# Kernel tuning notes

Hardware: AMD Instinct MI355X
Metric: run time of the kernel (lower is better)

## Reference

```python
import jax, jax.numpy as jnp
import numpy as np

B, N, MAX_DEG = 256, 512, 6
F_IN, H = 62, 128  # layers = [62, 128, 128]
NUM_DEG = MAX_DEG + 1  # degree buckets 0..6


def gather_neighbors(atoms, edges, maskvalue):
    # atoms [B,N,F], edges [B,N,D] with -1 padding -> [B,N,D,F]
    idx = jnp.maximum(edges, 0)
    neigh = jax.vmap(lambda a, e: a[e])(atoms, idx)
    return jnp.where(edges[..., None] < 0, jnp.asarray(maskvalue, atoms.dtype), neigh)


def nfp_conv(atoms, edges, W, b):
    # W [NUM_DEG, F_in, F_out], b [NUM_DEG, F_out]
    deg = jnp.sum(edges >= 0, axis=-1)  # [B,N]
    neigh = gather_neighbors(atoms, edges, 0.0)
    summed = neigh.sum(axis=2) + atoms  # include self, [B,N,F_in]
    out = jnp.zeros(summed.shape[:2] + (W.shape[-1],), summed.dtype)
    for d in range(NUM_DEG):  # small fixed set of degree buckets
        h = jax.nn.sigmoid(summed @ W[d] + b[d])
        out = out + h * (deg == d)[..., None].astype(h.dtype)
    return out


def graph_pool(atoms, edges):
    # max over self + neighbors
    neigh = gather_neighbors(atoms, edges, -jnp.inf)
    allf = jnp.concatenate([atoms[:, :, None, :], neigh], axis=2)  # [B,N,D+1,F]
    return allf.max(axis=2)


def setup_inputs() -> dict:
    key = jax.random.key(0)
    ka, ke, km, k0, k1, k2, k3 = jax.random.split(key, 7)
    a = jax.random.normal(ka, (B, N, F_IN), dtype=jnp.float32)
    e = jax.random.randint(ke, (B, N, MAX_DEG), 0, N, dtype=jnp.int32)
    # introduce -1 padding so atoms have varied degrees 0..6
    u = jax.random.uniform(km, (B, N, MAX_DEG))
    e = jnp.where(u < 0.6, e, -1).astype(jnp.int32)
    W0 = jax.random.normal(k0, (NUM_DEG, F_IN, H), dtype=jnp.float32) * 0.1
    b0 = jax.random.normal(k1, (NUM_DEG, H), dtype=jnp.float32) * 0.1
    W1 = jax.random.normal(k2, (NUM_DEG, H, H), dtype=jnp.float32) * 0.1
    b1 = jax.random.normal(k3, (NUM_DEG, H), dtype=jnp.float32) * 0.1
    return {"a": a, "e": e, "W0": W0, "b0": b0, "W1": W1, "b1": b1}


def reference(a, e, W0, b0, W1, b1):
    x = nfp_conv(a, e, W0, b0)
    x = graph_pool(x, e)
    x = nfp_conv(x, e, W1, b1)
    x = graph_pool(x, e)
    return x.sum(axis=1)  # SubgraphSum: [B, H]
```

## Files before the change

### kernel.cpp

```cpp
#include <hip/hip_runtime.h>
#include <math.h>

#define BB 256
#define NN 512
#define DD 6
#define F_IN 62
#define HH 128
#define ND 7
#define TOTAL (BB*NN)
#define OPB 640
#define GPB 40
#define TPB 10

typedef __bf16 bf16x8 __attribute__((ext_vector_type(8)));
typedef float f32x4 __attribute__((ext_vector_type(4)));

__device__ __forceinline__ unsigned short f2bf(float f) {
    unsigned u = __builtin_bit_cast(unsigned, f);
    u = (u + 0x7FFFu + ((u >> 16) & 1u)) >> 16;
    return (unsigned short)u;
}
__device__ __forceinline__ float lo2f(unsigned x) { return __builtin_bit_cast(float, x << 16); }
__device__ __forceinline__ float hi2f(unsigned x) { return __builtin_bit_cast(float, x & 0xFFFF0000u); }


__global__ __launch_bounds__(512) void k_sort16(const int* __restrict__ e,
                                                int* __restrict__ order,
                                                int* __restrict__ dgrp,
                                                int* __restrict__ ntiles) {
    __shared__ unsigned int scnt[ND];
    __shared__ unsigned int sbase[ND + 1];
    const int b = blockIdx.x;
    const int t = threadIdx.x;
    if (t < ND) scnt[t] = 0u;
    for (int i = t; i < OPB; i += 512) order[b * OPB + i] = -1;
    __syncthreads();
    int d = 0;
#pragma unroll
    for (int j = 0; j < DD; ++j) d += (e[(b * NN + t) * DD + j] >= 0) ? 1 : 0;
    unsigned rk = atomicAdd(&scnt[d], 1u);
    __syncthreads();
    if (t == 0) {
        unsigned acc = 0;
        for (int k = 0; k < ND; ++k) { sbase[k] = acc; acc += (scnt[k] + 15u) & ~15u; }
        sbase[ND] = acc;
        for (int k = 0; k < ND; ++k)
            for (unsigned g = sbase[k] >> 4; g < (sbase[k + 1] >> 4); ++g)
                dgrp[b * GPB + g] = k;
        for (unsigned g = acc >> 4; g < GPB; ++g) dgrp[b * GPB + g] = 0;
        ntiles[b] = (int)((acc + 63u) >> 6);
    }
    __syncthreads();
    order[b * OPB + sbase[d] + rk] = t;
}


__global__ __launch_bounds__(256) void k_prep_a(const float* __restrict__ a,
                                                unsigned short* __restrict__ Ap) {
    int u = blockIdx.x * 256 + threadIdx.x;
    int r = u >> 3;
    int c0 = (u & 7) * 8;
    unsigned short h[8];
#pragma unroll
    for (int i = 0; i < 8; ++i) {
        int c = c0 + i;
        h[i] = (c < F_IN) ? f2bf(a[(size_t)r * F_IN + c]) : (unsigned short)0;
    }
    uint4 p;
    p.x = (unsigned)h[0] | ((unsigned)h[1] << 16);
    p.y = (unsigned)h[2] | ((unsigned)h[3] << 16);
    p.z = (unsigned)h[4] | ((unsigned)h[5] << 16);
    p.w = (unsigned)h[6] | ((unsigned)h[7] << 16);
    *(uint4*)&Ap[(size_t)r * 64 + c0] = p;
}


__global__ void k_prep_wt(const float* __restrict__ W, unsigned short* __restrict__ WT,
                          int F, int K) {
    int n = blockIdx.x;
    int d = blockIdx.y;
    for (int k = threadIdx.x; k < K; k += 64) {
        float v = (k < F) ? W[((size_t)d * F + k) * HH + n] : 0.f;
        WT[((size_t)d * HH + n) * K + k] = f2bf(v);
    }
}


template<int KB>
__global__ __launch_bounds__(256, 3)
void k_conv_mfma(const unsigned short* __restrict__ Xp,
                 const int* __restrict__ e,
                 const unsigned short* __restrict__ WT,
                 const float* __restrict__ bias,
                 const int* __restrict__ order,
                 const int* __restrict__ dgrp,
                 const int* __restrict__ ntiles,
                 unsigned short* __restrict__ Y) {
    constexpr int K = KB * 8;
    constexpr int LOGKB = (KB == 16) ? 4 : 3;
    __shared__ unsigned short sP[64 * 128];
    __shared__ int vT[64];
    __shared__ int eT[64 * DD];

    const int t = threadIdx.x;
    const int l = t & 63;
    const int w = t >> 6;

    const int bi = blockIdx.x;
    const int x8 = bi & 7;
    const int j = bi >> 3;
    const int batch = x8 + 8 * (j / TPB);
    const int tile = j % TPB;
    if (tile >= ntiles[batch]) return;

    if (t < 64) vT[t] = order[batch * OPB + tile * 64 + t];
    __syncthreads();
    for (int i = t; i < 64 * DD; i += 256) {
        int v = vT[i / DD];
        if (v >= 0) eT[i] = e[((size_t)batch * NN + v) * DD + (i % DD)];
    }
    __syncthreads();

    for (int u = t; u < 64 * KB; u += 256) {
        const int kb = u & (KB - 1);
        const int n = u >> LOGKB;
        const int v = vT[n];
        float s[8] = {0.f, 0.f, 0.f, 0.f, 0.f, 0.f, 0.f, 0.f};
        if (v >= 0) {
            const unsigned short* base = Xp + (size_t)batch * NN * K;
            uint4 p = *(const uint4*)(base + (size_t)v * K + kb * 8);
            s[0] = lo2f(p.x); s[1] = hi2f(p.x); s[2] = lo2f(p.y); s[3] = hi2f(p.y);
            s[4] = lo2f(p.z); s[5] = hi2f(p.z); s[6] = lo2f(p.w); s[7] = hi2f(p.w);
#pragma unroll
            for (int jj = 0; jj < DD; ++jj) {
                int idx = eT[n * DD + jj];
                if (idx >= 0) {
                    uint4 q = *(const uint4*)(base + (size_t)idx * K + kb * 8);
                    s[0] += lo2f(q.x); s[1] += hi2f(q.x); s[2] += lo2f(q.y); s[3] += hi2f(q.y);
                    s[4] += lo2f(q.z); s[5] += hi2f(q.z); s[6] += lo2f(q.w); s[7] += hi2f(q.w);
                }
            }
        }
        uint4 r;
        r.x = (unsigned)f2bf(s[0]) | ((unsigned)f2bf(s[1]) << 16);
        r.y = (unsigned)f2bf(s[2]) | ((unsigned)f2bf(s[3]) << 16);
        r.z = (unsigned)f2bf(s[4]) | ((unsigned)f2bf(s[5]) << 16);
        r.w = (unsigned)f2bf(s[6]) | ((unsigned)f2bf(s[7]) << 16);
        const int kbs = kb ^ (n & 7);
        *(uint4*)&sP[(n * KB + kbs) * 8] = r;
    }
    __syncthreads();

    const int lr = l & 15;
    const int lq = l >> 4;

    int dg[4];
#pragma unroll
    for (int mb = 0; mb < 4; ++mb) dg[mb] = dgrp[batch * GPB + tile * 4 + mb];

    bf16x8 bf[K / 32][2];
    f32x4 acc[4][2];
    int dprev = -1;
#pragma unroll
    for (int mb = 0; mb < 4; ++mb) {
        const int d = dg[mb];
        if (d != dprev) {
#pragma unroll
            for (int kk = 0; kk < K / 32; ++kk)
#pragma unroll
                for (int nb = 0; nb < 2; ++nb) {
                    int ncol = w * 32 + nb * 16 + lr;
                    int krow = kk * 32 + lq * 8;
                    bf[kk][nb] = *(const bf16x8*)(WT + ((size_t)d * HH + ncol) * K + krow);
                }
            dprev = d;
        }
        f32x4 z0 = {0.f, 0.f, 0.f, 0.f};
        f32x4 z1 = {0.f, 0.f, 0.f, 0.f};
        const int nrow = mb * 16 + lr;
#pragma unroll
        for (int kk = 0; kk < K / 32; ++kk) {
            int kbp = kk * 4 + lq;
            int kbs = kbp ^ (nrow & 7);
            bf16x8 af = *(const bf16x8*)&sP[(nrow * KB + kbs) * 8];
            z0 = __builtin_amdgcn_mfma_f32_16x16x32_bf16(af, bf[kk][0], z0, 0, 0, 0);
            z1 = __builtin_amdgcn_mfma_f32_16x16x32_bf16(af, bf[kk][1], z1, 0, 0, 0);
        }
        acc[mb][0] = z0;
        acc[mb][1] = z1;
    }

    __syncthreads();
#pragma unroll
    for (int mb = 0; mb < 4; ++mb) {
        const int d = dg[mb];
#pragma unroll
        for (int nb = 0; nb < 2; ++nb) {
            int col = w * 32 + nb * 16 + lr;
            float bv = bias[d * HH + col];
#pragma unroll
            for (int r = 0; r < 4; ++r) {
                int n = mb * 16 + lq * 4 + r;
                float z = 1.f / (1.f + __expf(-(acc[mb][nb][r] + bv)));
                sP[n * HH + col] = f2bf(z);
            }
        }
    }
    __syncthreads();
    for (int u = t; u < 1024; u += 256) {
        int n = u >> 4;
        int c8 = (u & 15) * 8;
        int v = vT[n];
        if (v >= 0) {
            uint4 p = *(const uint4*)&sP[n * HH + c8];
            *(uint4*)&Y[((size_t)batch * NN + v) * HH + c8] = p;
        }
    }
}


__global__ __launch_bounds__(256) void k_pool_bf(const unsigned short* __restrict__ X,
                                                 const int* __restrict__ e,
                                                 unsigned short* __restrict__ P) {
    const int t = threadIdx.x;
    const int bi = blockIdx.x;
    const int x8 = bi & 7;
    const int j = bi >> 3;
    const int batch = x8 + 8 * (j >> 5);
    const int sub = j & 31;
    const int u = batch * NN + sub * 16 + (t >> 4);
    const int c8 = (t & 15) * 8;
    const int nbase = u & ~(NN - 1);
    float m[8];
    {
        uint4 p = *(const uint4*)(X + (size_t)u * HH + c8);
        m[0] = lo2f(p.x); m[1] = hi2f(p.x); m[2] = lo2f(p.y); m[3] = hi2f(p.y);
        m[4] = lo2f(p.z); m[5] = hi2f(p.z); m[6] = lo2f(p.w); m[7] = hi2f(p.w);
    }
#pragma unroll
    for (int jj = 0; jj < DD; ++jj) {
        int idx = e[u * DD + jj];
        if (idx >= 0) {
            uint4 p = *(const uint4*)(X + (size_t)(nbase + idx) * HH + c8);
            m[0] = fmaxf(m[0], lo2f(p.x)); m[1] = fmaxf(m[1], hi2f(p.x));
            m[2] = fmaxf(m[2], lo2f(p.y)); m[3] = fmaxf(m[3], hi2f(p.y));
            m[4] = fmaxf(m[4], lo2f(p.z)); m[5] = fmaxf(m[5], hi2f(p.z));
            m[6] = fmaxf(m[6], lo2f(p.w)); m[7] = fmaxf(m[7], hi2f(p.w));
        }
    }
    uint4 r;
    r.x = (unsigned)f2bf(m[0]) | ((unsigned)f2bf(m[1]) << 16);
    r.y = (unsigned)f2bf(m[2]) | ((unsigned)f2bf(m[3]) << 16);
    r.z = (unsigned)f2bf(m[4]) | ((unsigned)f2bf(m[5]) << 16);
    r.w = (unsigned)f2bf(m[6]) | ((unsigned)f2bf(m[7]) << 16);
    *(uint4*)&P[(size_t)u * HH + c8] = r;
}


__global__ __launch_bounds__(256) void k_pool_sum_part(const unsigned short* __restrict__ X,
                                                       const int* __restrict__ e,
                                                       float* __restrict__ partial) {
    __shared__ float red[16][HH + 4];
    const int t = threadIdx.x;
    const int bi = blockIdx.x;
    const int x8 = bi & 7;
    const int j = bi >> 3;
    const int b = x8 + 8 * (j >> 3);
    const int chunk = j & 7;
    const int slot = t >> 4;
    const int c8 = (t & 15) * 8;
    float acc[8];
#pragma unroll
    for (int i = 0; i < 8; ++i) acc[i] = 0.f;

    for (int n = chunk * 64 + slot; n < chunk * 64 + 64; n += 16) {
        int u = b * NN + n;
        float m[8];
        uint4 p = *(const uint4*)(X + (size_t)u * HH + c8);
        m[0] = lo2f(p.x); m[1] = hi2f(p.x); m[2] = lo2f(p.y); m[3] = hi2f(p.y);
        m[4] = lo2f(p.z); m[5] = hi2f(p.z); m[6] = lo2f(p.w); m[7] = hi2f(p.w);
#pragma unroll
        for (int jj = 0; jj < DD; ++jj) {
            int idx = e[u * DD + jj];
            if (idx >= 0) {
                uint4 q = *(const uint4*)(X + (size_t)(b * NN + idx) * HH + c8);
                m[0] = fmaxf(m[0], lo2f(q.x)); m[1] = fmaxf(m[1], hi2f(q.x));
                m[2] = fmaxf(m[2], lo2f(q.y)); m[3] = fmaxf(m[3], hi2f(q.y));
                m[4] = fmaxf(m[4], lo2f(q.z)); m[5] = fmaxf(m[5], hi2f(q.z));
                m[6] = fmaxf(m[6], lo2f(q.w)); m[7] = fmaxf(m[7], hi2f(q.w));
            }
        }
#pragma unroll
        for (int i = 0; i < 8; ++i) acc[i] += m[i];
    }
#pragma unroll
    for (int i = 0; i < 8; ++i) red[slot][c8 + i] = acc[i];
    __syncthreads();
    if (t < HH) {
        float s = 0.f;
#pragma unroll
        for (int k = 0; k < 16; ++k) s += red[k][t];
        partial[(size_t)(b * 8 + chunk) * HH + t] = s;
    }
}


__global__ __launch_bounds__(256) void k_sum_final(const float* __restrict__ partial,
                                                   float* __restrict__ out) {
    int g = blockIdx.x * 256 + threadIdx.x;
    int b = g >> 7;
    int c = g & 127;
    float s = 0.f;
#pragma unroll
    for (int k = 0; k < 8; ++k) s += partial[(size_t)(b * 8 + k) * HH + c];
    out[g] = s;
}


extern "C" void kernel_launch(void* const* d_in, const int* in_sizes, int n_in,
                              void* d_out, int out_size, void* d_ws, size_t ws_size,
                              hipStream_t stream) {
    const float* a  = (const float*)d_in[0];
    const int*   e  = (const int*)d_in[1];
    const float* W0 = (const float*)d_in[2];
    const float* b0 = (const float*)d_in[3];
    const float* W1 = (const float*)d_in[4];
    const float* b1 = (const float*)d_in[5];
    float* out = (float*)d_out;

    char* ws = (char*)d_ws;
    const size_t XB = (size_t)TOTAL * HH * 2;
    unsigned short* xbuf = (unsigned short*)ws;
    unsigned short* pbuf = (unsigned short*)(ws + XB);
    unsigned short* Ap   = (unsigned short*)(ws + 2 * XB);
    float* partial = (float*)Ap;
    unsigned short* WT0  = (unsigned short*)(ws + 2 * XB + (size_t)TOTAL * 64 * 2);
    unsigned short* WT1  = WT0 + (size_t)ND * HH * 64;
    char* ip = (char*)(WT1 + (size_t)ND * HH * 128);
    int* order  = (int*)ip;
    int* dgrp   = (int*)(ip + (size_t)BB * OPB * 4);
    int* ntiles = (int*)(ip + (size_t)BB * (OPB + GPB) * 4);

    hipLaunchKernelGGL(k_sort16, dim3(BB), dim3(NN), 0, stream, e, order, dgrp, ntiles);

    hipLaunchKernelGGL(k_prep_a, dim3(TOTAL * 8 / 256), dim3(256), 0, stream, a, Ap);
    hipLaunchKernelGGL(k_prep_wt, dim3(HH, ND), dim3(64), 0, stream, W0, WT0, F_IN, 64);
    hipLaunchKernelGGL(k_prep_wt, dim3(HH, ND), dim3(64), 0, stream, W1, WT1, HH, HH);

    hipLaunchKernelGGL((k_conv_mfma<8>),  dim3(BB * TPB), dim3(256), 0, stream,
                       Ap, e, WT0, b0, order, dgrp, ntiles, xbuf);
    hipLaunchKernelGGL(k_pool_bf, dim3(TOTAL / 16), dim3(256), 0, stream, xbuf, e, pbuf);
    hipLaunchKernelGGL((k_conv_mfma<16>), dim3(BB * TPB), dim3(256), 0, stream,
                       pbuf, e, WT1, b1, order, dgrp, ntiles, xbuf);
    hipLaunchKernelGGL(k_pool_sum_part, dim3(BB * 8), dim3(256), 0, stream, xbuf, e, partial);
    hipLaunchKernelGGL(k_sum_final, dim3(BB * HH / 256), dim3(256), 0, stream, partial, out);
}
```

Before: 146.5 us.

## Widen conv blocks to one wave per row-block slice and split pool-sum finer

The MFMA conv kernel now runs with 512 or 1024 threads per block. Each thread gathers exactly one neighbor-sum element, and each wave computes one 16-row block over a slice of output columns, with its A fragments preloaded from LDS. Previously each wave looped over all four row blocks and cached weights in registers. The pool-sum kernel gives each thread a single node and uses 32 partial chunks per graph instead of 8, and the final reduction sums 32 partials. The aim is more parallelism and latency hiding in the gather-heavy phases, at the cost of reloading weights per wave and tighter register limits from the launch bounds of 8.

```diff
diff --git a/kernel.cpp b/kernel.cpp
--- a/kernel.cpp
+++ b/kernel.cpp
@@ -86,8 +86,8 @@
 }
 
 
-template<int KB>
-__global__ __launch_bounds__(256, 3)
+template<int KB, int THREADS>
+__global__ __launch_bounds__(THREADS, 8)
 void k_conv_mfma(const unsigned short* __restrict__ Xp,
                  const int* __restrict__ e,
                  const unsigned short* __restrict__ WT,
@@ -98,6 +98,10 @@
                  unsigned short* __restrict__ Y) {
     constexpr int K = KB * 8;
     constexpr int LOGKB = (KB == 16) ? 4 : 3;
+    constexpr int WAVES = THREADS / 64;
+    constexpr int SUBW = WAVES / 4;
+    constexpr int CPW = 128 / SUBW;
+    constexpr int NFR = CPW / 16;
     __shared__ unsigned short sP[64 * 128];
     __shared__ int vT[64];
     __shared__ int eT[64 * DD];
@@ -115,27 +119,27 @@
 
     if (t < 64) vT[t] = order[batch * OPB + tile * 64 + t];
     __syncthreads();
-    for (int i = t; i < 64 * DD; i += 256) {
-        int v = vT[i / DD];
-        if (v >= 0) eT[i] = e[((size_t)batch * NN + v) * DD + (i % DD)];
-    }
-    __syncthreads();
-
-    for (int u = t; u < 64 * KB; u += 256) {
-        const int kb = u & (KB - 1);
-        const int n = u >> LOGKB;
+    if (t < 64 * DD) {
+        int v = vT[t / DD];
+        eT[t] = (v >= 0) ? e[((size_t)batch * NN + v) * DD + (t % DD)] : -1;
+    }
+    __syncthreads();
+
+    {
+        const int kb = t & (KB - 1);
+        const int n = t >> LOGKB;
         const int v = vT[n];
         float s[8] = {0.f, 0.f, 0.f, 0.f, 0.f, 0.f, 0.f, 0.f};
         if (v >= 0) {
-            const unsigned short* base = Xp + (size_t)batch * NN * K;
-            uint4 p = *(const uint4*)(base + (size_t)v * K + kb * 8);
+            const unsigned short* base = Xp + (size_t)batch * NN * K + kb * 8;
+            uint4 p = *(const uint4*)(base + (size_t)v * K);
             s[0] = lo2f(p.x); s[1] = hi2f(p.x); s[2] = lo2f(p.y); s[3] = hi2f(p.y);
             s[4] = lo2f(p.z); s[5] = hi2f(p.z); s[6] = lo2f(p.w); s[7] = hi2f(p.w);
 #pragma unroll
             for (int jj = 0; jj < DD; ++jj) {
                 int idx = eT[n * DD + jj];
                 if (idx >= 0) {
-                    uint4 q = *(const uint4*)(base + (size_t)idx * K + kb * 8);
+                    uint4 q = *(const uint4*)(base + (size_t)idx * K);
                     s[0] += lo2f(q.x); s[1] += hi2f(q.x); s[2] += lo2f(q.y); s[3] += hi2f(q.y);
                     s[4] += lo2f(q.z); s[5] += hi2f(q.z); s[6] += lo2f(q.w); s[7] += hi2f(q.w);
                 }
@@ -146,68 +150,49 @@
         r.y = (unsigned)f2bf(s[2]) | ((unsigned)f2bf(s[3]) << 16);
         r.z = (unsigned)f2bf(s[4]) | ((unsigned)f2bf(s[5]) << 16);
         r.w = (unsigned)f2bf(s[6]) | ((unsigned)f2bf(s[7]) << 16);
-        const int kbs = kb ^ (n & 7);
-        *(uint4*)&sP[(n * KB + kbs) * 8] = r;
+        *(uint4*)&sP[(n * KB + (kb ^ (n & 7))) * 8] = r;
     }
     __syncthreads();
 
     const int lr = l & 15;
     const int lq = l >> 4;
-
-    int dg[4];
-#pragma unroll
-    for (int mb = 0; mb < 4; ++mb) dg[mb] = dgrp[batch * GPB + tile * 4 + mb];
-
-    bf16x8 bf[K / 32][2];
-    f32x4 acc[4][2];
-    int dprev = -1;
-#pragma unroll
-    for (int mb = 0; mb < 4; ++mb) {
-        const int d = dg[mb];
-        if (d != dprev) {
-#pragma unroll
-            for (int kk = 0; kk < K / 32; ++kk)
-#pragma unroll
-                for (int nb = 0; nb < 2; ++nb) {
-                    int ncol = w * 32 + nb * 16 + lr;
-                    int krow = kk * 32 + lq * 8;
-                    bf[kk][nb] = *(const bf16x8*)(WT + ((size_t)d * HH + ncol) * K + krow);
-                }
-            dprev = d;
-        }
-        f32x4 z0 = {0.f, 0.f, 0.f, 0.f};
-        f32x4 z1 = {0.f, 0.f, 0.f, 0.f};
-        const int nrow = mb * 16 + lr;
+    const int mb = w / SUBW;
+    const int col0 = (w % SUBW) * CPW;
+    const int d = dgrp[batch * GPB + tile * 4 + mb];
+    const int nrow = mb * 16 + lr;
+
+    bf16x8 af[K / 32];
+#pragma unroll
+    for (int kk = 0; kk < K / 32; ++kk)
+        af[kk] = *(const bf16x8*)&sP[(nrow * KB + ((kk * 4 + lq) ^ (nrow & 7))) * 8];
+
+    f32x4 acc[NFR];
+#pragma unroll
+    for (int fr = 0; fr < NFR; ++fr) { f32x4 z = {0.f, 0.f, 0.f, 0.f}; acc[fr] = z; }
+#pragma unroll
+    for (int fr = 0; fr < NFR; ++fr) {
+        const unsigned short* wp = WT + ((size_t)d * HH + col0 + fr * 16 + lr) * K + lq * 8;
 #pragma unroll
         for (int kk = 0; kk < K / 32; ++kk) {
-            int kbp = kk * 4 + lq;
-            int kbs = kbp ^ (nrow & 7);
-            bf16x8 af = *(const bf16x8*)&sP[(nrow * KB + kbs) * 8];
-            z0 = __builtin_amdgcn_mfma_f32_16x16x32_bf16(af, bf[kk][0], z0, 0, 0, 0);
-            z1 = __builtin_amdgcn_mfma_f32_16x16x32_bf16(af, bf[kk][1], z1, 0, 0, 0);
-        }
-        acc[mb][0] = z0;
-        acc[mb][1] = z1;
-    }
-
-    __syncthreads();
-#pragma unroll
-    for (int mb = 0; mb < 4; ++mb) {
-        const int d = dg[mb];
-#pragma unroll
-        for (int nb = 0; nb < 2; ++nb) {
-            int col = w * 32 + nb * 16 + lr;
-            float bv = bias[d * HH + col];
-#pragma unroll
-            for (int r = 0; r < 4; ++r) {
-                int n = mb * 16 + lq * 4 + r;
-                float z = 1.f / (1.f + __expf(-(acc[mb][nb][r] + bv)));
-                sP[n * HH + col] = f2bf(z);
-            }
-        }
-    }
-    __syncthreads();
-    for (int u = t; u < 1024; u += 256) {
+            bf16x8 bfr = *(const bf16x8*)(wp + kk * 32);
+            acc[fr] = __builtin_amdgcn_mfma_f32_16x16x32_bf16(af[kk], bfr, acc[fr], 0, 0, 0);
+        }
+    }
+
+    __syncthreads();
+#pragma unroll
+    for (int fr = 0; fr < NFR; ++fr) {
+        const int col = col0 + fr * 16 + lr;
+        const float bv = bias[d * HH + col];
+#pragma unroll
+        for (int r = 0; r < 4; ++r) {
+            const int n = mb * 16 + lq * 4 + r;
+            float z = 1.f / (1.f + __expf(-(acc[fr][r] + bv)));
+            sP[n * HH + col] = f2bf(z);
+        }
+    }
+    __syncthreads();
+    for (int u = t; u < 1024; u += THREADS) {
         int n = u >> 4;
         int c8 = (u & 15) * 8;
         int v = vT[n];
@@ -265,42 +250,37 @@
     const int bi = blockIdx.x;
     const int x8 = bi & 7;
     const int j = bi >> 3;
-    const int b = x8 + 8 * (j >> 3);
-    const int chunk = j & 7;
+    const int b = x8 + 8 * (j >> 5);
+    const int chunk = j & 31;
     const int slot = t >> 4;
     const int c8 = (t & 15) * 8;
-    float acc[8];
-#pragma unroll
-    for (int i = 0; i < 8; ++i) acc[i] = 0.f;
-
-    for (int n = chunk * 64 + slot; n < chunk * 64 + 64; n += 16) {
-        int u = b * NN + n;
-        float m[8];
+
+    const int u = b * NN + chunk * 16 + slot;
+    float m[8];
+    {
         uint4 p = *(const uint4*)(X + (size_t)u * HH + c8);
         m[0] = lo2f(p.x); m[1] = hi2f(p.x); m[2] = lo2f(p.y); m[3] = hi2f(p.y);
         m[4] = lo2f(p.z); m[5] = hi2f(p.z); m[6] = lo2f(p.w); m[7] = hi2f(p.w);
-#pragma unroll
-        for (int jj = 0; jj < DD; ++jj) {
-            int idx = e[u * DD + jj];
-            if (idx >= 0) {
-                uint4 q = *(const uint4*)(X + (size_t)(b * NN + idx) * HH + c8);
-                m[0] = fmaxf(m[0], lo2f(q.x)); m[1] = fmaxf(m[1], hi2f(q.x));
-                m[2] = fmaxf(m[2], lo2f(q.y)); m[3] = fmaxf(m[3], hi2f(q.y));
-                m[4] = fmaxf(m[4], lo2f(q.z)); m[5] = fmaxf(m[5], hi2f(q.z));
-                m[6] = fmaxf(m[6], lo2f(q.w)); m[7] = fmaxf(m[7], hi2f(q.w));
-            }
-        }
-#pragma unroll
-        for (int i = 0; i < 8; ++i) acc[i] += m[i];
-    }
-#pragma unroll
-    for (int i = 0; i < 8; ++i) red[slot][c8 + i] = acc[i];
+    }
+#pragma unroll
+    for (int jj = 0; jj < DD; ++jj) {
+        int idx = e[u * DD + jj];
+        if (idx >= 0) {
+            uint4 q = *(const uint4*)(X + (size_t)(b * NN + idx) * HH + c8);
+            m[0] = fmaxf(m[0], lo2f(q.x)); m[1] = fmaxf(m[1], hi2f(q.x));
+            m[2] = fmaxf(m[2], lo2f(q.y)); m[3] = fmaxf(m[3], hi2f(q.y));
+            m[4] = fmaxf(m[4], lo2f(q.z)); m[5] = fmaxf(m[5], hi2f(q.z));
+            m[6] = fmaxf(m[6], lo2f(q.w)); m[7] = fmaxf(m[7], hi2f(q.w));
+        }
+    }
+#pragma unroll
+    for (int i = 0; i < 8; ++i) red[slot][c8 + i] = m[i];
     __syncthreads();
     if (t < HH) {
         float s = 0.f;
 #pragma unroll
         for (int k = 0; k < 16; ++k) s += red[k][t];
-        partial[(size_t)(b * 8 + chunk) * HH + t] = s;
+        partial[((size_t)b * 32 + chunk) * HH + t] = s;
     }
 }
 
@@ -312,7 +292,7 @@
     int c = g & 127;
     float s = 0.f;
 #pragma unroll
-    for (int k = 0; k < 8; ++k) s += partial[(size_t)(b * 8 + k) * HH + c];
+    for (int k = 0; k < 32; ++k) s += partial[((size_t)b * 32 + k) * HH + c];
     out[g] = s;
 }
 
@@ -347,11 +327,11 @@
     hipLaunchKernelGGL(k_prep_wt, dim3(HH, ND), dim3(64), 0, stream, W0, WT0, F_IN, 64);
     hipLaunchKernelGGL(k_prep_wt, dim3(HH, ND), dim3(64), 0, stream, W1, WT1, HH, HH);
 
-    hipLaunchKernelGGL((k_conv_mfma<8>),  dim3(BB * TPB), dim3(256), 0, stream,
+    hipLaunchKernelGGL((k_conv_mfma<8, 512>),   dim3(BB * TPB), dim3(512), 0, stream,
                        Ap, e, WT0, b0, order, dgrp, ntiles, xbuf);
     hipLaunchKernelGGL(k_pool_bf, dim3(TOTAL / 16), dim3(256), 0, stream, xbuf, e, pbuf);
-    hipLaunchKernelGGL((k_conv_mfma<16>), dim3(BB * TPB), dim3(256), 0, stream,
+    hipLaunchKernelGGL((k_conv_mfma<16, 1024>), dim3(BB * TPB), dim3(1024), 0, stream,
                        pbuf, e, WT1, b1, order, dgrp, ntiles, xbuf);
-    hipLaunchKernelGGL(k_pool_sum_part, dim3(BB * 8), dim3(256), 0, stream, xbuf, e, partial);
+    hipLaunchKernelGGL(k_pool_sum_part, dim3(BB * 32), dim3(256), 0, stream, xbuf, e, partial);
     hipLaunchKernelGGL(k_sum_final, dim3(BB * HH / 256), dim3(256), 0, stream, partial, out);
 }
```

New measurement: 169.8 us. 16.0% more time.
